# Optimization experiments

Measured on AMD Instinct MI355X. Metric: run time of the kernel, lower is better.

Reference implementation:

```python
import jax, jax.numpy as jnp
import numpy as np

B, S, D, H = 2, 4096, 1024, 16
DK = D // H


def setup_inputs() -> dict:
    key = jax.random.key(0)
    ks = jax.random.split(key, 8)
    q = jax.random.normal(ks[0], (B, S, D), dtype=jnp.float32)
    k = jax.random.normal(ks[1], (B, S, D), dtype=jnp.float32)
    v = jax.random.normal(ks[2], (B, S, D), dtype=jnp.float32)
    mask = jax.random.randint(ks[3], (1, 1, S, S), 0, 2, dtype=jnp.int32)
    # torch.nn.Linear weights, y = x @ W.T ; Kaiming-uniform-ish init scale
    lim = 1.0 / np.sqrt(D)
    Wq = jax.random.uniform(ks[4], (D, D), jnp.float32, -lim, lim)
    Wk = jax.random.uniform(ks[5], (D, D), jnp.float32, -lim, lim)
    Wv = jax.random.uniform(ks[6], (D, D), jnp.float32, -lim, lim)
    Wo = jax.random.uniform(ks[7], (D, D), jnp.float32, -lim, lim)
    return {"q": q, "k": k, "v": v, "mask": mask,
            "Wq": Wq, "Wk": Wk, "Wv": Wv, "Wo": Wo}


def reference(q, k, v, mask, Wq, Wk, Wv, Wo):
    # Linear projections (torch Linear: x @ W.T), split into heads [B,H,S,DK]
    def heads(x, W):
        return (x @ W.T).reshape(B, S, H, DK).transpose(0, 2, 1, 3)

    Q, K, V = heads(q, Wq), heads(k, Wk), heads(v, Wv)
    scale = 1.0 / jnp.sqrt(jnp.asarray(DK, dtype=Q.dtype))
    # [B,H,S,S] score matrix (original materializes it fully)
    scores = jnp.einsum("bhqd,bhkd->bhqk", Q, K) * scale
    # NOTE: original calls masked_fill without assignment -> mask is a no-op.
    # Dropout: eval-mode identity (original also references missing self.dropout).
    attn = jax.nn.softmax(scores, axis=-1)
    out = jnp.einsum("bhqk,bhkd->bhqd", attn, V)  # [B,H,S,DK]
    out = out.transpose(0, 2, 1, 3).reshape(B, S, D)
    return out @ Wo.T
```

## Files before the change

kernel.cpp:

```cpp
#include <hip/hip_runtime.h>
#include <cstdint>
#include <cstddef>

using u16 = unsigned short;
using u32 = unsigned int;

typedef _Float16 f16x8 __attribute__((ext_vector_type(8)));
typedef float    f32x4 __attribute__((ext_vector_type(4)));
typedef float    f32x16 __attribute__((ext_vector_type(16)));

#define MFMA16(a,b,c) __builtin_amdgcn_mfma_f32_16x16x32_f16((a),(b),(c),0,0,0)
#define MFMA32(a,b,c) __builtin_amdgcn_mfma_f32_32x32x16_f16((a),(b),(c),0,0,0)

__device__ __forceinline__ u16 f2h(float f) {
  return __builtin_bit_cast(u16, (_Float16)f);
}
__device__ __forceinline__ u32 pkrtz(float a, float b) {
  return __builtin_bit_cast(u32, __builtin_amdgcn_cvt_pkrtz(a, b));
}
__device__ __forceinline__ void plswap(u32 &a, u32 &b) {
  asm volatile("v_permlane32_swap_b32 %0, %1" : "+v"(a), "+v"(b));
}
__device__ __forceinline__ void async16(const void* g, void* lds) {
  __builtin_amdgcn_global_load_lds((const __attribute__((address_space(1))) void*)g,
                                   (__attribute__((address_space(3))) void*)lds,
                                   16, 0, 0);
}
#if __has_builtin(__builtin_amdgcn_exp2f)
__device__ __forceinline__ float exp2_hw(float x) { return __builtin_amdgcn_exp2f(x); }
#else
__device__ __forceinline__ float exp2_hw(float x) {
  float r; asm("v_exp_f32 %0, %1" : "=v"(r) : "v"(x)); return r;
}
#endif

__global__ __launch_bounds__(256) void cvt4_w(const float* __restrict__ w0,
                                              const float* __restrict__ w1,
                                              const float* __restrict__ w2,
                                              const float* __restrict__ w3,
                                              u16* __restrict__ d0, u16* __restrict__ d1,
                                              u16* __restrict__ d2, u16* __restrict__ d3,
                                              int n4, float scale0) {
  const int y = blockIdx.y;
  const float* in = y == 0 ? w0 : (y == 1 ? w1 : (y == 2 ? w2 : w3));
  u16* out = y == 0 ? d0 : (y == 1 ? d1 : (y == 2 ? d2 : d3));
  const float sc = y == 0 ? scale0 : 1.0f;
  int i = blockIdx.x * 256 + threadIdx.x;
  const int stride = gridDim.x * 256;
  for (; i < n4; i += stride) {
    const float4 f = reinterpret_cast<const float4*>(in)[i];
    ushort4 o;
    o.x = f2h(f.x * sc); o.y = f2h(f.y * sc);
    o.z = f2h(f.z * sc); o.w = f2h(f.w * sc);
    reinterpret_cast<ushort4*>(out)[i] = o;
  }
}

__global__ __launch_bounds__(256) void cvt3_x(const float* __restrict__ q,
                                              const float* __restrict__ k,
                                              const float* __restrict__ v,
                                              u16* __restrict__ xq, u16* __restrict__ xk,
                                              u16* __restrict__ xv, int n4) {
  const int y = blockIdx.y;
  const float* in = y == 0 ? q : (y == 1 ? k : v);
  u16* out = y == 0 ? xq : (y == 1 ? xk : xv);
  int i = blockIdx.x * 256 + threadIdx.x;
  const int stride = gridDim.x * 256;
  for (; i < n4; i += stride) {
    const float4 f = reinterpret_cast<const float4*>(in)[i];
    ushort4 o;
    o.x = f2h(f.x); o.y = f2h(f.y); o.z = f2h(f.z); o.w = f2h(f.w);
    reinterpret_cast<ushort4*>(out)[i] = o;
  }
}

template <int OF32>
__device__ __forceinline__ void gemm_body(const u16* __restrict__ A,
                                          const u16* __restrict__ Bw,
                                          float* __restrict__ Cf,
                                          u16* __restrict__ Ch,
                                          int m0, int n0, int N, int K) {
  __shared__ __align__(16) u16 Asm[128 * 64];
  __shared__ __align__(16) u16 Bsm[128 * 64];
  const int tid = threadIdx.x;
  const int w = tid >> 6, l = tid & 63;
  const int wr = w >> 1, wc = w & 1;
  const int lr = l >> 3, lc = l & 7, csrc = lc ^ lr;
  const int laneq = l & 15, laneg = l >> 4;
  f32x4 acc[4][4] = {};
  for (int k0 = 0; k0 < K; k0 += 64) {
    __syncthreads();
#pragma unroll
    for (int c = 0; c < 4; ++c) {
      const int row = c * 32 + w * 8 + lr;
      async16(A + (size_t)(m0 + row) * K + k0 + csrc * 8, &Asm[c * 2048 + w * 512]);
      async16(Bw + (size_t)(n0 + row) * K + k0 + csrc * 8, &Bsm[c * 2048 + w * 512]);
    }
    __syncthreads();
#pragma unroll
    for (int ks = 0; ks < 2; ++ks) {
      f16x8 af[4], bfr[4];
#pragma unroll
      for (int mi = 0; mi < 4; ++mi) {
        const int row = wr * 64 + mi * 16 + laneq;
        const int ch = (ks * 4 + laneg) ^ (row & 7);
        af[mi] = *(const f16x8*)&Asm[row * 64 + ch * 8];
      }
#pragma unroll
      for (int ni = 0; ni < 4; ++ni) {
        const int row = wc * 64 + ni * 16 + laneq;
        const int ch = (ks * 4 + laneg) ^ (row & 7);
        bfr[ni] = *(const f16x8*)&Bsm[row * 64 + ch * 8];
      }
#pragma unroll
      for (int mi = 0; mi < 4; ++mi)
#pragma unroll
        for (int ni = 0; ni < 4; ++ni)
          acc[mi][ni] = MFMA16(af[mi], bfr[ni], acc[mi][ni]);
    }
  }
#pragma unroll
  for (int mi = 0; mi < 4; ++mi)
#pragma unroll
    for (int r = 0; r < 4; ++r) {
      const int gm = m0 + wr * 64 + mi * 16 + laneg * 4 + r;
#pragma unroll
      for (int ni = 0; ni < 4; ++ni) {
        const int gn = n0 + wc * 64 + ni * 16 + laneq;
        if constexpr (OF32) Cf[(size_t)gm * N + gn] = acc[mi][ni][r];
        else                Ch[(size_t)gm * N + gn] = f2h(acc[mi][ni][r]);
      }
    }
}

__global__ __launch_bounds__(256) void gemm_qkv(const u16* __restrict__ xq,
                                                const u16* __restrict__ wq,
                                                u16* __restrict__ Qp,
                                                const u16* __restrict__ xk,
                                                const u16* __restrict__ wk,
                                                u16* __restrict__ Kp,
                                                const u16* __restrict__ xv,
                                                const u16* __restrict__ wv,
                                                u16* __restrict__ VT) {
  const int z = blockIdx.z;
  if (z == 2) {
    gemm_body<0>(wv, xv, nullptr, VT, blockIdx.x * 128, blockIdx.y * 128, 8192, 1024);
  } else {
    const bool zk = z != 0;
    gemm_body<0>(zk ? xk : xq, zk ? wk : wq, nullptr, zk ? Kp : Qp,
                 blockIdx.y * 128, blockIdx.x * 128, 1024, 1024);
  }
}

__global__ __launch_bounds__(256) void gemm_f(const u16* __restrict__ A,
                                              const u16* __restrict__ Bw,
                                              float* __restrict__ Cf,
                                              int N, int K) {
  gemm_body<1>(A, Bw, Cf, nullptr, blockIdx.y * 128, blockIdx.x * 128, N, K);
}

__global__ __launch_bounds__(256, 4) void attn_fwd(const u16* __restrict__ Qp,
                                                   const u16* __restrict__ Kp,
                                                   const u16* __restrict__ VT,
                                                   u16* __restrict__ AO) {
  union SM {
    struct { u16 K[2][64 * 64]; u16 V[2][64 * 64]; } st;
    u16 osm[4][32 * 72];
  };
  __shared__ __align__(16) SM sm;
  const int tid = threadIdx.x, w = tid >> 6, l = tid & 63;
  const int l31 = l & 31, hi = l >> 5, l7 = l & 7, lr = l >> 3;
  const int bid = blockIdx.x;
  const int slot = bid >> 3;
  const int bh = (bid & 7) * 4 + (slot >> 5), qx = slot & 31;
  const int b = bh >> 4, h = bh & 15;
  const int q0 = qx * 128;
  const size_t hb = (size_t)b * 4096 * 1024 + (size_t)h * 64;
  const u16* Kh = Kp + hb;
  const u16* Vh = VT + (size_t)h * 64 * 8192 + (size_t)b * 4096;
  const int csrc = l7 ^ lr;

  f16x8 qf[4];
  {
    const u16* qp = Qp + hb + (size_t)(q0 + w * 32 + l31) * 1024 + hi * 8;
#pragma unroll
    for (int kk = 0; kk < 4; ++kk) qf[kk] = *(const f16x8*)(qp + kk * 16);
  }

  f32x16 zero16;
#pragma unroll
  for (int r = 0; r < 16; ++r) zero16[r] = 0.f;
  f16x8 ones;
#pragma unroll
  for (int r = 0; r < 8; ++r) ones[r] = (_Float16)1.0f;

  f32x16 acc[2];
  f32x16 accl;
#pragma unroll
  for (int r = 0; r < 16; ++r) { acc[0][r] = 0.f; acc[1][r] = 0.f; accl[r] = 0.f; }

  int koff = (w * 8 + lr) * 1024 + csrc * 8;
  int voff = (w * 8 + lr) * 8192 + csrc * 8;

  async16(Kh + koff,             &sm.st.K[0][w * 512]);
  async16(Kh + koff + 32 * 1024, &sm.st.K[0][w * 512 + 2048]);
  async16(Vh + voff,             &sm.st.V[0][w * 512]);
  async16(Vh + voff + 32 * 8192, &sm.st.V[0][w * 512 + 2048]);

  for (int t = 0; t < 64; ++t) {
    const int cur = t & 1;
    __syncthreads();
    if (t < 63) {
      koff += 64 * 1024;
      voff += 64;
      async16(Kh + koff,             &sm.st.K[cur ^ 1][w * 512]);
      async16(Kh + koff + 32 * 1024, &sm.st.K[cur ^ 1][w * 512 + 2048]);
      async16(Vh + voff,             &sm.st.V[cur ^ 1][w * 512]);
      async16(Vh + voff + 32 * 8192, &sm.st.V[cur ^ 1][w * 512 + 2048]);
    }
    const u16* Ks = sm.st.K[cur];
    const u16* Vs = sm.st.V[cur];

    __builtin_amdgcn_s_setprio(1);
    f32x16 sv;
    {
      f16x8 kf = *(const f16x8*)&Ks[l31 * 64 + ((hi ^ l7) << 3)];
      sv = MFMA32(kf, qf[0], zero16);
#pragma unroll
      for (int kk = 1; kk < 4; ++kk) {
        kf = *(const f16x8*)&Ks[l31 * 64 + (((kk * 2 + hi) ^ l7) << 3)];
        sv = MFMA32(kf, qf[kk], sv);
      }
    }
    __builtin_amdgcn_s_setprio(0);
#pragma unroll
    for (int r = 0; r < 16; ++r) sv[r] = exp2_hw(sv[r]);
    f16x8 pf0[2];
#pragma unroll
    for (int half = 0; half < 2; ++half) {
      const int rb = half * 8;
      u32 a0 = pkrtz(sv[rb + 0], sv[rb + 1]);
      u32 a1 = pkrtz(sv[rb + 2], sv[rb + 3]);
      u32 b0 = pkrtz(sv[rb + 4], sv[rb + 5]);
      u32 b1 = pkrtz(sv[rb + 6], sv[rb + 7]);
      plswap(a0, b0);
      plswap(a1, b1);
      union { u32 ww[4]; f16x8 v; } uu;
      uu.ww[0] = a0; uu.ww[1] = a1; uu.ww[2] = b0; uu.ww[3] = b1;
      pf0[half] = uu.v;
    }
    __builtin_amdgcn_s_setprio(1);
    {
      f16x8 kf = *(const f16x8*)&Ks[(32 + l31) * 64 + ((hi ^ l7) << 3)];
      sv = MFMA32(kf, qf[0], zero16);
#pragma unroll
      for (int kk = 1; kk < 4; ++kk) {
        kf = *(const f16x8*)&Ks[(32 + l31) * 64 + (((kk * 2 + hi) ^ l7) << 3)];
        sv = MFMA32(kf, qf[kk], sv);
      }
    }
    __builtin_amdgcn_sched_barrier(0);
#pragma unroll
    for (int half = 0; half < 2; ++half) {
      accl = MFMA32(ones, pf0[half], accl);
#pragma unroll
      for (int ds = 0; ds < 2; ++ds) {
        const f16x8 vf = *(const f16x8*)&Vs[(ds * 32 + l31) * 64 + (((half * 2 + hi) ^ l7) << 3)];
        acc[ds] = MFMA32(vf, pf0[half], acc[ds]);
      }
    }
    __builtin_amdgcn_s_setprio(0);
#pragma unroll
    for (int r = 0; r < 16; ++r) sv[r] = exp2_hw(sv[r]);
    f16x8 pf1[2];
#pragma unroll
    for (int half = 0; half < 2; ++half) {
      const int rb = half * 8;
      u32 a0 = pkrtz(sv[rb + 0], sv[rb + 1]);
      u32 a1 = pkrtz(sv[rb + 2], sv[rb + 3]);
      u32 b0 = pkrtz(sv[rb + 4], sv[rb + 5]);
      u32 b1 = pkrtz(sv[rb + 6], sv[rb + 7]);
      plswap(a0, b0);
      plswap(a1, b1);
      union { u32 ww[4]; f16x8 v; } uu;
      uu.ww[0] = a0; uu.ww[1] = a1; uu.ww[2] = b0; uu.ww[3] = b1;
      pf1[half] = uu.v;
    }
    __builtin_amdgcn_s_setprio(1);
#pragma unroll
    for (int half = 0; half < 2; ++half) {
      accl = MFMA32(ones, pf1[half], accl);
#pragma unroll
      for (int ds = 0; ds < 2; ++ds) {
        const f16x8 vf = *(const f16x8*)&Vs[(ds * 32 + l31) * 64 + (((4 + half * 2 + hi) ^ l7) << 3)];
        acc[ds] = MFMA32(vf, pf1[half], acc[ds]);
      }
    }
    __builtin_amdgcn_s_setprio(0);
  }
  __syncthreads();
  {
    const float rn = 1.f / accl[0];
#pragma unroll
    for (int ds = 0; ds < 2; ++ds)
#pragma unroll
      for (int g = 0; g < 4; ++g) {
        uint2 val;
        val.x = pkrtz(acc[ds][4 * g + 0] * rn, acc[ds][4 * g + 1] * rn);
        val.y = pkrtz(acc[ds][4 * g + 2] * rn, acc[ds][4 * g + 3] * rn);
        *(uint2*)&sm.osm[w][l31 * 72 + ds * 32 + g * 8 + hi * 4] = val;
      }
  }
  asm volatile("s_waitcnt lgkmcnt(0)" ::: "memory");
#pragma unroll
  for (int i = 0; i < 4; ++i) {
    const int row = lr + i * 8;
    const uint4 vv = *(const uint4*)&sm.osm[w][row * 72 + l7 * 8];
    *(uint4*)(AO + hb + (size_t)(q0 + w * 32 + row) * 1024 + l7 * 8) = vv;
  }
}

extern "C" void kernel_launch(void* const* d_in, const int* in_sizes, int n_in,
                              void* d_out, int out_size, void* d_ws, size_t ws_size,
                              hipStream_t stream) {
  const float* q  = (const float*)d_in[0];
  const float* k  = (const float*)d_in[1];
  const float* v  = (const float*)d_in[2];
  const float* Wq = (const float*)d_in[4];
  const float* Wk = (const float*)d_in[5];
  const float* Wv = (const float*)d_in[6];
  const float* Wo = (const float*)d_in[7];
  float* out = (float*)d_out;

  char* ws = (char*)d_ws;
  u16* xq  = (u16*)ws;
  u16* xk  = (u16*)(ws + 16777216);
  u16* xv  = (u16*)(ws + 2 * 16777216);
  u16* Qp  = (u16*)(ws + 3 * 16777216);
  u16* Kpp = (u16*)(ws + 4 * 16777216);
  u16* wqb = (u16*)(ws + 5 * 16777216);
  u16* wkb = wqb + 1048576;
  u16* wvb = wkb + 1048576;
  u16* wob = wvb + 1048576;
  u16* VT  = xq;
  u16* AO  = xv;

  constexpr float SC = 0.125f * 1.44269504088896340736f;
  cvt4_w<<<dim3(256, 4), 256, 0, stream>>>(Wq, Wk, Wv, Wo, wqb, wkb, wvb, wob,
                                           262144, SC);
  cvt3_x<<<dim3(1024, 3), 256, 0, stream>>>(q, k, v, xq, xk, xv, 2097152);

  gemm_qkv<<<dim3(8, 64, 3), 256, 0, stream>>>(xq, wqb, Qp, xk, wkb, Kpp,
                                               xv, wvb, VT);

  attn_fwd<<<1024, 256, 0, stream>>>(Qp, Kpp, VT, AO);

  gemm_f<<<dim3(8, 64), 256, 0, stream>>>(AO, wob, out, 1024, 1024);
}
```

Baseline: 283.6 us.

## Replace ones-MFMA row sum with VALU sums and hand-schedule attention loop

The softmax denominator is now accumulated with VALU adds and a cross-half shuffle instead of extra MFMAs against a ones vector. This removes four MFMAs per iteration from the matrix pipe. The first QK MFMA block is moved ahead of the next tile's async loads, and sched_group_barrier directives interleave MFMA, VALU and LDS reads explicitly. The fused QKV projection launch is also split into separate QK and V^T launches. The trade-off is extra VALU work and more rigid compiler scheduling.

Measured after the change: 276.5 us. 1.03x faster.

```diff
diff --git a/kernel.cpp b/kernel.cpp
--- a/kernel.cpp
+++ b/kernel.cpp
@@ -11,6 +11,7 @@
 
 #define MFMA16(a,b,c) __builtin_amdgcn_mfma_f32_16x16x32_f16((a),(b),(c),0,0,0)
 #define MFMA32(a,b,c) __builtin_amdgcn_mfma_f32_32x32x16_f16((a),(b),(c),0,0,0)
+#define SGB __builtin_amdgcn_sched_group_barrier
 
 __device__ __forceinline__ u16 f2h(float f) {
   return __builtin_bit_cast(u16, (_Float16)f);
@@ -133,23 +134,21 @@
     }
 }
 
-__global__ __launch_bounds__(256) void gemm_qkv(const u16* __restrict__ xq,
-                                                const u16* __restrict__ wq,
-                                                u16* __restrict__ Qp,
-                                                const u16* __restrict__ xk,
-                                                const u16* __restrict__ wk,
-                                                u16* __restrict__ Kp,
-                                                const u16* __restrict__ xv,
-                                                const u16* __restrict__ wv,
-                                                u16* __restrict__ VT) {
-  const int z = blockIdx.z;
-  if (z == 2) {
-    gemm_body<0>(wv, xv, nullptr, VT, blockIdx.x * 128, blockIdx.y * 128, 8192, 1024);
-  } else {
-    const bool zk = z != 0;
-    gemm_body<0>(zk ? xk : xq, zk ? wk : wq, nullptr, zk ? Kp : Qp,
-                 blockIdx.y * 128, blockIdx.x * 128, 1024, 1024);
-  }
+__global__ __launch_bounds__(256) void gemm_qk(const u16* __restrict__ xq,
+                                               const u16* __restrict__ wq,
+                                               u16* __restrict__ Qp,
+                                               const u16* __restrict__ xk,
+                                               const u16* __restrict__ wk,
+                                               u16* __restrict__ Kp) {
+  const bool zk = blockIdx.z != 0;
+  gemm_body<0>(zk ? xk : xq, zk ? wk : wq, nullptr, zk ? Kp : Qp,
+               blockIdx.y * 128, blockIdx.x * 128, 1024, 1024);
+}
+
+__global__ __launch_bounds__(256) void gemm_vt(const u16* __restrict__ wv,
+                                               const u16* __restrict__ xv,
+                                               u16* __restrict__ VT) {
+  gemm_body<0>(wv, xv, nullptr, VT, blockIdx.y * 128, blockIdx.x * 128, 8192, 1024);
 }
 
 __global__ __launch_bounds__(256) void gemm_f(const u16* __restrict__ A,
@@ -190,14 +189,11 @@
   f32x16 zero16;
 #pragma unroll
   for (int r = 0; r < 16; ++r) zero16[r] = 0.f;
-  f16x8 ones;
-#pragma unroll
-  for (int r = 0; r < 8; ++r) ones[r] = (_Float16)1.0f;
 
   f32x16 acc[2];
-  f32x16 accl;
-#pragma unroll
-  for (int r = 0; r < 16; ++r) { acc[0][r] = 0.f; acc[1][r] = 0.f; accl[r] = 0.f; }
+#pragma unroll
+  for (int r = 0; r < 16; ++r) { acc[0][r] = 0.f; acc[1][r] = 0.f; }
+  float lp0 = 0.f, lp1 = 0.f, lp2 = 0.f, lp3 = 0.f;
 
   int koff = (w * 8 + lr) * 1024 + csrc * 8;
   int voff = (w * 8 + lr) * 8192 + csrc * 8;
@@ -210,6 +206,21 @@
   for (int t = 0; t < 64; ++t) {
     const int cur = t & 1;
     __syncthreads();
+    const u16* Ks = sm.st.K[cur];
+    const u16* Vs = sm.st.V[cur];
+
+    __builtin_amdgcn_s_setprio(1);
+    f32x16 sv;
+    {
+      f16x8 kf = *(const f16x8*)&Ks[l31 * 64 + ((hi ^ l7) << 3)];
+      sv = MFMA32(kf, qf[0], zero16);
+#pragma unroll
+      for (int kk = 1; kk < 4; ++kk) {
+        kf = *(const f16x8*)&Ks[l31 * 64 + (((kk * 2 + hi) ^ l7) << 3)];
+        sv = MFMA32(kf, qf[kk], sv);
+      }
+    }
+    __builtin_amdgcn_s_setprio(0);
     if (t < 63) {
       koff += 64 * 1024;
       voff += 64;
@@ -218,24 +229,14 @@
       async16(Vh + voff,             &sm.st.V[cur ^ 1][w * 512]);
       async16(Vh + voff + 32 * 8192, &sm.st.V[cur ^ 1][w * 512 + 2048]);
     }
-    const u16* Ks = sm.st.K[cur];
-    const u16* Vs = sm.st.V[cur];
-
-    __builtin_amdgcn_s_setprio(1);
-    f32x16 sv;
-    {
-      f16x8 kf = *(const f16x8*)&Ks[l31 * 64 + ((hi ^ l7) << 3)];
-      sv = MFMA32(kf, qf[0], zero16);
-#pragma unroll
-      for (int kk = 1; kk < 4; ++kk) {
-        kf = *(const f16x8*)&Ks[l31 * 64 + (((kk * 2 + hi) ^ l7) << 3)];
-        sv = MFMA32(kf, qf[kk], sv);
-      }
-    }
-    __builtin_amdgcn_s_setprio(0);
+
+    f16x8 pf0[2];
 #pragma unroll
     for (int r = 0; r < 16; ++r) sv[r] = exp2_hw(sv[r]);
-    f16x8 pf0[2];
+    lp0 += sv[0] + sv[4];  lp1 += sv[1] + sv[5];
+    lp2 += sv[2] + sv[6];  lp3 += sv[3] + sv[7];
+    lp0 += sv[8] + sv[12]; lp1 += sv[9] + sv[13];
+    lp2 += sv[10] + sv[14]; lp3 += sv[11] + sv[15];
 #pragma unroll
     for (int half = 0; half < 2; ++half) {
       const int rb = half * 8;
@@ -249,7 +250,7 @@
       uu.ww[0] = a0; uu.ww[1] = a1; uu.ww[2] = b0; uu.ww[3] = b1;
       pf0[half] = uu.v;
     }
-    __builtin_amdgcn_s_setprio(1);
+
     {
       f16x8 kf = *(const f16x8*)&Ks[(32 + l31) * 64 + ((hi ^ l7) << 3)];
       sv = MFMA32(kf, qf[0], zero16);
@@ -259,20 +260,22 @@
         sv = MFMA32(kf, qf[kk], sv);
       }
     }
-    __builtin_amdgcn_sched_barrier(0);
-#pragma unroll
-    for (int half = 0; half < 2; ++half) {
-      accl = MFMA32(ones, pf0[half], accl);
+
+#pragma unroll
+    for (int half = 0; half < 2; ++half)
 #pragma unroll
       for (int ds = 0; ds < 2; ++ds) {
         const f16x8 vf = *(const f16x8*)&Vs[(ds * 32 + l31) * 64 + (((half * 2 + hi) ^ l7) << 3)];
         acc[ds] = MFMA32(vf, pf0[half], acc[ds]);
       }
-    }
-    __builtin_amdgcn_s_setprio(0);
+
+    f16x8 pf1[2];
 #pragma unroll
     for (int r = 0; r < 16; ++r) sv[r] = exp2_hw(sv[r]);
-    f16x8 pf1[2];
+    lp0 += sv[0] + sv[4];  lp1 += sv[1] + sv[5];
+    lp2 += sv[2] + sv[6];  lp3 += sv[3] + sv[7];
+    lp0 += sv[8] + sv[12]; lp1 += sv[9] + sv[13];
+    lp2 += sv[10] + sv[14]; lp3 += sv[11] + sv[15];
 #pragma unroll
     for (int half = 0; half < 2; ++half) {
       const int rb = half * 8;
@@ -286,21 +289,29 @@
       uu.ww[0] = a0; uu.ww[1] = a1; uu.ww[2] = b0; uu.ww[3] = b1;
       pf1[half] = uu.v;
     }
-    __builtin_amdgcn_s_setprio(1);
-#pragma unroll
-    for (int half = 0; half < 2; ++half) {
-      accl = MFMA32(ones, pf1[half], accl);
+
+#pragma unroll
+    for (int half = 0; half < 2; ++half)
 #pragma unroll
       for (int ds = 0; ds < 2; ++ds) {
         const f16x8 vf = *(const f16x8*)&Vs[(ds * 32 + l31) * 64 + (((4 + half * 2 + hi) ^ l7) << 3)];
         acc[ds] = MFMA32(vf, pf1[half], acc[ds]);
       }
-    }
-    __builtin_amdgcn_s_setprio(0);
-  }
+
+    SGB(0x2, 72, 0);
+    SGB(0x8, 4, 0);
+    SGB(0x100, 2, 0); SGB(0x8, 1, 0); SGB(0x2, 18, 0);
+    SGB(0x100, 2, 0); SGB(0x8, 1, 0); SGB(0x2, 18, 0);
+    SGB(0x8, 1, 0);   SGB(0x2, 18, 0);
+    SGB(0x8, 1, 0);   SGB(0x2, 18, 0);
+    SGB(0x100, 4, 0);
+    SGB(0x8, 4, 0);
+  }
+  float ls = (lp0 + lp1) + (lp2 + lp3);
+  ls += __shfl_xor(ls, 32);
   __syncthreads();
   {
-    const float rn = 1.f / accl[0];
+    const float rn = 1.f / ls;
 #pragma unroll
     for (int ds = 0; ds < 2; ++ds)
 #pragma unroll
@@ -350,8 +361,8 @@
                                            262144, SC);
   cvt3_x<<<dim3(1024, 3), 256, 0, stream>>>(q, k, v, xq, xk, xv, 2097152);
 
-  gemm_qkv<<<dim3(8, 64, 3), 256, 0, stream>>>(xq, wqb, Qp, xk, wkb, Kpp,
-                                               xv, wvb, VT);
+  gemm_qk<<<dim3(8, 64, 2), 256, 0, stream>>>(xq, wqb, Qp, xk, wkb, Kpp);
+  gemm_vt<<<dim3(64, 8), 256, 0, stream>>>(wvb, xv, VT);
 
   attn_fwd<<<1024, 256, 0, stream>>>(Qp, Kpp, VT, AO);
 
```
